# Performance work log

Hardware: AMD Instinct MI355X
Metric: run time of the kernel (lower is better)

The kernel has to match this reference:

```python
import jax, jax.numpy as jnp
import numpy as np

H, DH, DIM = 6, 13, 78   # heads, dim_head, model dim
LA, LG = 1.0, 0.5        # La (softmax scale), Lg (adjacency weight)
B, N = 16, 512


def setup_inputs() -> dict:
    key = jax.random.key(0)
    ks = jax.random.split(key, 5)
    x = jax.random.normal(ks[0], (B, N, DIM), jnp.float32)
    mask = jax.random.randint(ks[1], (B, N), 0, 2).astype(bool)
    adjacency_mat = jax.random.uniform(ks[2], (B, N, N), jnp.float32)
    # to_qkv: Linear(dim, 3*h*d, bias=False); to_out: Linear(h*d, dim)
    W_qkv = jax.random.normal(ks[3], (DIM, H * 3 * DH), jnp.float32) * 0.05
    W_out = jax.random.normal(ks[4], (H * DH, DIM), jnp.float32) * 0.05
    b_out = jnp.zeros((DIM,), jnp.float32)
    return {"x": x, "mask": mask, "adjacency_mat": adjacency_mat,
            "W_qkv": W_qkv, "W_out": W_out, "b_out": b_out}


def reference(x, mask, adjacency_mat, W_qkv, W_out, b_out):
    b, n, _ = x.shape
    # rearrange 'b n (h qkv d) -> b h n qkv d': inner dim split as (h, 3, d)
    qkv = (x @ W_qkv).reshape(b, n, H, 3, DH)
    qkv = jnp.transpose(qkv, (0, 2, 1, 3, 4))            # b h n 3 d
    q, k, v = qkv[..., 0, :], qkv[..., 1, :], qkv[..., 2, :]
    scale = DH ** -0.5
    dots = jnp.einsum('bhid,bhjd->bhij', q, k) * scale   # b h n n
    m = mask[:, None, :, None] & mask[:, None, None, :]  # b 1 n n
    big = jnp.finfo(dots.dtype).max
    dots = jnp.where(m, dots, -big)                      # masked_fill_(~mask, -max)
    adj = jnp.where(m, adjacency_mat[:, None, :, :], 0.0)
    attn = jax.nn.softmax(dots, axis=-1) * LA + LG * adj
    out = jnp.einsum('bhij,bhjd->bhid', attn, v)         # b h n d
    out = jnp.transpose(out, (0, 2, 1, 3)).reshape(b, n, H * DH)
    return out @ W_out + b_out
```

## Files before the change

kernel.cpp:

```cpp
#include <hip/hip_runtime.h>
#include <hip/hip_bf16.h>
#include <cfloat>

#define BB 16
#define NN 512
#define DIMX 78
#define NH 6
#define DHH 13
#define QS 16
#define KS 16
#define NC (NH*3*DHH)
#define SCALE 0.27735009811261457f
#define LAM_A 1.0f
#define LAM_G 0.5f
#define NU 32

typedef unsigned short ushortx;
typedef ushortx ushort8 __attribute__((ext_vector_type(8)));
typedef _Float16 halfx;
typedef halfx half2v __attribute__((ext_vector_type(2)));

__device__ __forceinline__ ushortx f2h(float f) {
  halfx h = (halfx)f;
  return __builtin_bit_cast(unsigned short, h);
}
__device__ __forceinline__ float h2lo(unsigned d) {
  return (float)__builtin_bit_cast(half2v, d).x;
}
__device__ __forceinline__ float h2hi(unsigned d) {
  return (float)__builtin_bit_cast(half2v, d).y;
}

__device__ __forceinline__ float dot2acc(unsigned qd, unsigned kd, float c) {
#if __has_builtin(__builtin_amdgcn_fdot2)
  return __builtin_amdgcn_fdot2(__builtin_bit_cast(half2v, qd),
                                __builtin_bit_cast(half2v, kd), c, false);
#else
  half2v qa = __builtin_bit_cast(half2v, qd);
  half2v ka = __builtin_bit_cast(half2v, kd);
  c = fmaf((float)qa.x, (float)ka.x, c);
  return fmaf((float)qa.y, (float)ka.y, c);
#endif
}

__global__ __launch_bounds__(256) void qkv_kernel(
    const float* __restrict__ x, const float* __restrict__ Wqkv,
    ushortx* __restrict__ qh, ushortx* __restrict__ kh, ushortx* __restrict__ vh) {
  int idx = blockIdx.x * 256 + threadIdx.x;
  const int NQ = 59;
  int rq = idx / NQ, cq = idx % NQ;
  if (rq >= (BB * NN) / 4) return;
  int c0 = cq * 4; if (c0 > NC - 4) c0 = NC - 4;
  int r0 = rq * 4;
  const float* x0 = x + (size_t)r0 * DIMX;
  const float* wb = Wqkv + c0;

  float acc[4][4];
#pragma unroll
  for (int r = 0; r < 4; ++r)
#pragma unroll
    for (int c = 0; c < 4; ++c) acc[r][c] = 0.f;

#pragma unroll 2
  for (int d0 = 0; d0 < 76; d0 += 4) {
    float2 wA[4], wB[4];
#pragma unroll
    for (int dd = 0; dd < 4; ++dd) {
      wA[dd] = *(const float2*)(wb + (d0 + dd) * NC);
      wB[dd] = *(const float2*)(wb + (d0 + dd) * NC + 2);
    }
    float2 xv[4][2];
#pragma unroll
    for (int r = 0; r < 4; ++r) {
      xv[r][0] = *(const float2*)(x0 + r * DIMX + d0);
      xv[r][1] = *(const float2*)(x0 + r * DIMX + d0 + 2);
    }
#pragma unroll
    for (int dd = 0; dd < 4; ++dd) {
#pragma unroll
      for (int r = 0; r < 4; ++r) {
        float xvv = (dd < 2) ? ((dd & 1) ? xv[r][0].y : xv[r][0].x)
                             : ((dd & 1) ? xv[r][1].y : xv[r][1].x);
        acc[r][0] = fmaf(xvv, wA[dd].x, acc[r][0]);
        acc[r][1] = fmaf(xvv, wA[dd].y, acc[r][1]);
        acc[r][2] = fmaf(xvv, wB[dd].x, acc[r][2]);
        acc[r][3] = fmaf(xvv, wB[dd].y, acc[r][3]);
      }
    }
  }
#pragma unroll
  for (int dd = 0; dd < 2; ++dd) {
    int d = 76 + dd;
    float2 wA = *(const float2*)(wb + d * NC);
    float2 wB = *(const float2*)(wb + d * NC + 2);
#pragma unroll
    for (int r = 0; r < 4; ++r) {
      float xvv = x0[r * DIMX + d];
      acc[r][0] = fmaf(xvv, wA.x, acc[r][0]);
      acc[r][1] = fmaf(xvv, wA.y, acc[r][1]);
      acc[r][2] = fmaf(xvv, wB.x, acc[r][2]);
      acc[r][3] = fmaf(xvv, wB.y, acc[r][3]);
    }
  }

#pragma unroll
  for (int r = 0; r < 4; ++r) {
    int bn = r0 + r;
    int b = bn / NN, n = bn % NN;
#pragma unroll
    for (int c = 0; c < 4; ++c) {
      int col = c0 + c;
      int h  = col / (3 * DHH);
      int rm = col % (3 * DHH);
      int t  = rm / DHH;
      int dd = rm % DHH;
      size_t rowb = ((size_t)b * NH + h) * NN + n;
      if (t == 0)      qh[rowb * QS + dd] = f2h(acc[r][c] * SCALE);
      else if (t == 1) kh[rowb * KS + dd] = f2h(acc[r][c]);
      else             vh[rowb * KS + dd] = f2h(acc[r][c]);
    }
  }
}

__global__ __launch_bounds__(256, 4) void attn_kernel(
    const ushortx* __restrict__ qh, const ushortx* __restrict__ kh,
    const ushortx* __restrict__ vh, const int* __restrict__ mask,
    const float* __restrict__ adj, float* __restrict__ att) {
  __shared__ uint4 k0s[NN], k1s[NN];
  __shared__ uint4 v0s[NN], v1s[NN];
  __shared__ __align__(16) unsigned qs[64][8];
  __shared__ short jact[NN];
  __shared__ unsigned char ract[64];
  __shared__ float vsum[DHH];
  __shared__ float vpart_s[2][DHH];
  __shared__ int nact_s, nract_s;

  int d0    = blockIdx.x;
  int orig  = (d0 & 7) * 96 + (d0 >> 3);
  int itile = orig & 7;
  int bh    = orig >> 3;
  int b     = bh / NH;
  int h     = bh % NH;
  int i0    = itile * 64;

  const ushortx* qb  = qh + (size_t)bh * NN * QS;
  const ushortx* kbb = kh + (size_t)bh * NN * KS;
  const ushortx* vbb = vh + (size_t)bh * NN * KS;
  const int* mrow = mask + b * NN;

  int tid  = threadIdx.x;
  int wave = tid >> 6, lane = tid & 63;

  if (wave == 0) {
    unsigned m8 = 0;
#pragma unroll
    for (int t = 0; t < 8; ++t) {
      int j = lane * 8 + t;
      if (mrow[j] != 0) m8 |= (1u << t);
    }
    int cnt = __popc(m8);
    int pre = cnt;
#pragma unroll
    for (int off = 1; off < 64; off <<= 1) {
      int o = __shfl_up(pre, off);
      if (lane >= off) pre += o;
    }
    pre -= cnt;
    int w = pre;
#pragma unroll
    for (int t = 0; t < 8; ++t)
      if ((m8 >> t) & 1) jact[w++] = (short)(lane * 8 + t);
    if (lane == 63) nact_s = pre + cnt;
  } else if (wave == 1) {
    int a = (mrow[i0 + lane] != 0) ? 1 : 0;
    int pre = a;
#pragma unroll
    for (int off = 1; off < 64; off <<= 1) {
      int o = __shfl_up(pre, off);
      if (lane >= off) pre += o;
    }
    pre -= a;
    if (a) ract[pre] = (unsigned char)lane;
    if (lane == 63) nract_s = pre + a;
  } else {
    int idx2 = (wave - 2) * 64 + lane;
    float vp[DHH];
#pragma unroll
    for (int d = 0; d < DHH; ++d) vp[d] = 0.f;
#pragma unroll
    for (int rep = 0; rep < 4; ++rep) {
      const ushortx* vr = vbb + (size_t)(idx2 + rep * 128) * KS;
      uint4 f0 = *(const uint4*)(vr);
      uint4 f1 = *(const uint4*)(vr + 8);
      vp[0] += h2lo(f0.x); vp[1] += h2hi(f0.x);
      vp[2] += h2lo(f0.y); vp[3] += h2hi(f0.y);
      vp[4] += h2lo(f0.z); vp[5] += h2hi(f0.z);
      vp[6] += h2lo(f0.w); vp[7] += h2hi(f0.w);
      vp[8] += h2lo(f1.x); vp[9] += h2hi(f1.x);
      vp[10] += h2lo(f1.y); vp[11] += h2hi(f1.y);
      vp[12] += h2lo(f1.z);
    }
#pragma unroll
    for (int off = 1; off < 64; off <<= 1)
#pragma unroll
      for (int d = 0; d < DHH; ++d) vp[d] += __shfl_xor(vp[d], off);
    if (lane < DHH) vpart_s[wave - 2][lane] = vp[lane];
  }
  __syncthreads();

  int na = nact_s;
  int nr = nract_s;

  {
    int r = tid >> 2, c2 = (tid & 3) * 2;
    *(uint2*)&qs[r][c2] = *(const uint2*)(qb + (size_t)(i0 + r) * QS + c2 * 2);
  }
  for (int t = tid; t < NN; t += 256) {
    if (t < na) {
      int j = jact[t];
      const ushortx* kr = kbb + (size_t)j * KS;
      const ushortx* vr = vbb + (size_t)j * KS;
      uint4 ka = *(const uint4*)(kr);
      uint4 kc = *(const uint4*)(kr + 8);
      kc.z &= 0xFFFFu;
      kc.w = 0;
      k0s[t] = ka;
      k1s[t] = kc;
      v0s[t] = *(const uint4*)(vr);
      v1s[t] = *(const uint4*)(vr + 8);
    } else {
      uint4 z = make_uint4(0, 0, 0, 0);
      k0s[t] = z; k1s[t] = z; v0s[t] = z; v1s[t] = z;
      jact[t] = 0;
    }
  }
  if (tid < DHH) vsum[tid] = vpart_s[0][tid] + vpart_s[1][tid];
  __syncthreads();

  for (int e = tid; e < 64 * DHH; e += 256) {
    int r = e / DHH, d = e % DHH;
    int i = i0 + r;
    if (mrow[i] == 0)
      att[((size_t)b * NN + i) * DIMX + h * DHH + d] = (LAM_A / 512.f) * vsum[d];
  }

  int grp = lane >> 4;
  int li  = lane & 15;

  for (int base = wave * 4; base < nr; base += 16) {
    int ridx = base + grp;
    bool rok = ridx < nr;
    int rl = ract[rok ? ridx : 0];
    int i  = i0 + rl;
    unsigned qd[7];
#pragma unroll
    for (int p = 0; p < 7; ++p) qd[p] = qs[rl][p];
    const float* adjr = adj + ((size_t)b * NN + i) * NN;

    float s[NU], aj[NU];
    float sum = 0.f;
#pragma unroll
    for (int u = 0; u < NU; ++u) {
      if (u * 16 < na) {
        int t = u * 16 + li;
        uint4 ka = k0s[t];
        uint4 kc = k1s[t];
        aj[u] = adjr[jact[t]];
        float dot = dot2acc(qd[0], ka.x, 0.f);
        dot = dot2acc(qd[1], ka.y, dot);
        dot = dot2acc(qd[2], ka.z, dot);
        dot = dot2acc(qd[3], ka.w, dot);
        dot = dot2acc(qd[4], kc.x, dot);
        dot = dot2acc(qd[5], kc.y, dot);
        dot = dot2acc(qd[6], kc.z, dot);
        float p = __expf((t < na) ? dot : -FLT_MAX);
        s[u] = p;
        sum += p;
      }
    }
#pragma unroll
    for (int off = 1; off < 16; off <<= 1) sum += __shfl_xor(sum, off);
    float inv = LAM_A / sum;

    float acc[DHH];
#pragma unroll
    for (int d = 0; d < DHH; ++d) acc[d] = 0.f;
#pragma unroll
    for (int u = 0; u < NU; ++u) {
      if (u * 16 < na) {
        int t = u * 16 + li;
        uint4 va = v0s[t];
        uint4 vc = v1s[t];
        float wu = fmaf(LAM_G, aj[u], s[u] * inv);
        acc[0]  = fmaf(h2lo(va.x), wu, acc[0]);
        acc[1]  = fmaf(h2hi(va.x), wu, acc[1]);
        acc[2]  = fmaf(h2lo(va.y), wu, acc[2]);
        acc[3]  = fmaf(h2hi(va.y), wu, acc[3]);
        acc[4]  = fmaf(h2lo(va.z), wu, acc[4]);
        acc[5]  = fmaf(h2hi(va.z), wu, acc[5]);
        acc[6]  = fmaf(h2lo(va.w), wu, acc[6]);
        acc[7]  = fmaf(h2hi(va.w), wu, acc[7]);
        acc[8]  = fmaf(h2lo(vc.x), wu, acc[8]);
        acc[9]  = fmaf(h2hi(vc.x), wu, acc[9]);
        acc[10] = fmaf(h2lo(vc.y), wu, acc[10]);
        acc[11] = fmaf(h2hi(vc.y), wu, acc[11]);
        acc[12] = fmaf(h2lo(vc.z), wu, acc[12]);
      }
    }
#pragma unroll
    for (int off = 1; off < 16; off <<= 1) {
#pragma unroll
      for (int d = 0; d < DHH; ++d) acc[d] += __shfl_xor(acc[d], off);
    }

    if (rok && li == 0) {
#pragma unroll
      for (int d = 0; d < DHH; ++d)
        att[((size_t)b * NN + i) * DIMX + h * DHH + d] = acc[d];
    }
  }
}

__global__ __launch_bounds__(320) void proj_kernel(
    const float* __restrict__ att, const float* __restrict__ Wout,
    const float* __restrict__ bout, float* __restrict__ out) {
  __shared__ float Ws[DIMX][80];
  __shared__ float as[32][82];
  __shared__ float bs[80];
  int tid = threadIdx.x;
  for (int e = tid; e < DIMX * 80; e += 320) {
    int r = e / 80, c = e % 80;
    Ws[r][c] = (c < DIMX) ? Wout[r * DIMX + c] : 0.f;
  }
  if (tid < 80) bs[tid] = (tid < DIMX) ? bout[tid] : 0.f;
  size_t row0 = (size_t)blockIdx.x * 32;
  for (int e = tid; e < 32 * DIMX; e += 320)
    as[e / DIMX][e % DIMX] = att[row0 * DIMX + e];
  __syncthreads();

  int r2 = tid / 20;
  int cq = tid % 20;
  int c0 = cq * 4;
  float acc0[4], acc1[4];
#pragma unroll
  for (int kk = 0; kk < 4; ++kk) { acc0[kk] = bs[c0 + kk]; acc1[kk] = bs[c0 + kk]; }

#pragma unroll 6
  for (int d = 0; d < DIMX; ++d) {
    float4 w = *(const float4*)&Ws[d][c0];
    float a0 = as[r2 * 2 + 0][d];
    float a1 = as[r2 * 2 + 1][d];
    acc0[0] = fmaf(a0, w.x, acc0[0]); acc0[1] = fmaf(a0, w.y, acc0[1]);
    acc0[2] = fmaf(a0, w.z, acc0[2]); acc0[3] = fmaf(a0, w.w, acc0[3]);
    acc1[0] = fmaf(a1, w.x, acc1[0]); acc1[1] = fmaf(a1, w.y, acc1[1]);
    acc1[2] = fmaf(a1, w.z, acc1[2]); acc1[3] = fmaf(a1, w.w, acc1[3]);
  }

  size_t r0o = (row0 + r2 * 2) * (size_t)DIMX;
  *(float2*)&out[r0o + c0]        = make_float2(acc0[0], acc0[1]);
  *(float2*)&out[r0o + DIMX + c0] = make_float2(acc1[0], acc1[1]);
  if (cq < 19) {
    *(float2*)&out[r0o + c0 + 2]        = make_float2(acc0[2], acc0[3]);
    *(float2*)&out[r0o + DIMX + c0 + 2] = make_float2(acc1[2], acc1[3]);
  }
}

extern "C" void kernel_launch(void* const* d_in, const int* in_sizes, int n_in,
                              void* d_out, int out_size, void* d_ws, size_t ws_size,
                              hipStream_t stream) {
  const float* x    = (const float*)d_in[0];
  const int*   mask = (const int*)d_in[1];
  const float* adj  = (const float*)d_in[2];
  const float* Wqkv = (const float*)d_in[3];
  const float* Wout = (const float*)d_in[4];
  const float* bout = (const float*)d_in[5];
  float* out = (float*)d_out;

  const size_t heads_rows = (size_t)BB * NH * NN;
  float*   att = (float*)d_ws;
  ushortx* qhp = (ushortx*)(att + (size_t)BB * NN * DIMX);
  ushortx* khp = qhp + heads_rows * QS;
  ushortx* vhp = khp + heads_rows * KS;

  const int NQ = 59;
  int qkv_threads = (BB * NN / 4) * NQ;
  qkv_kernel<<<(qkv_threads + 255) / 256, 256, 0, stream>>>(x, Wqkv, qhp, khp, vhp);
  attn_kernel<<<BB * NH * (NN / 64), 256, 0, stream>>>(qhp, khp, vhp, mask, adj, att);
  proj_kernel<<<BB * NN / 32, 320, 0, stream>>>(att, Wout, bout, out);
}
```

Before: 52.97 us.

## Fuse output projection into attention kernel via per-head atomic accumulation

Removes the separate projection kernel. The qkv kernel now also initializes the output with the bias, and each attention block multiplies its per-head 64x13 result by that head's slice of W_out and atomically adds it into the output. Fully masked rows use a precomputed projected mean-V vector. This drops the att intermediate round trip through global memory and one launch. In exchange it adds float atomics from 6 heads per output element, makes summation order nondeterministic, and lowers the occupancy hint to 3.

```diff
diff --git a/kernel.cpp b/kernel.cpp
--- a/kernel.cpp
+++ b/kernel.cpp
@@ -45,8 +45,13 @@
 
 __global__ __launch_bounds__(256) void qkv_kernel(
     const float* __restrict__ x, const float* __restrict__ Wqkv,
-    ushortx* __restrict__ qh, ushortx* __restrict__ kh, ushortx* __restrict__ vh) {
+    const float* __restrict__ bout,
+    ushortx* __restrict__ qh, ushortx* __restrict__ kh, ushortx* __restrict__ vh,
+    float* __restrict__ out) {
   int idx = blockIdx.x * 256 + threadIdx.x;
+  for (int e = idx; e < BB * NN * DIMX; e += gridDim.x * 256)
+    out[e] = bout[e % DIMX];
+
   const int NQ = 59;
   int rq = idx / NQ, cq = idx % NQ;
   if (rq >= (BB * NN) / 4) return;
@@ -122,13 +127,17 @@
   }
 }
 
-__global__ __launch_bounds__(256, 4) void attn_kernel(
+__global__ __launch_bounds__(256, 3) void attn_kernel(
     const ushortx* __restrict__ qh, const ushortx* __restrict__ kh,
     const ushortx* __restrict__ vh, const int* __restrict__ mask,
-    const float* __restrict__ adj, float* __restrict__ att) {
+    const float* __restrict__ adj, const float* __restrict__ Wout,
+    float* __restrict__ out) {
   __shared__ uint4 k0s[NN], k1s[NN];
   __shared__ uint4 v0s[NN], v1s[NN];
   __shared__ __align__(16) unsigned qs[64][8];
+  __shared__ float att_s[64][14];
+  __shared__ float Ws2[DHH][80];
+  __shared__ float uv[80];
   __shared__ short jact[NN];
   __shared__ unsigned char ract[64];
   __shared__ float vsum[DHH];
@@ -214,6 +223,10 @@
   {
     int r = tid >> 2, c2 = (tid & 3) * 2;
     *(uint2*)&qs[r][c2] = *(const uint2*)(qb + (size_t)(i0 + r) * QS + c2 * 2);
+  }
+  for (int e = tid; e < DHH * 80; e += 256) {
+    int r = e / 80, c = e % 80;
+    Ws2[r][c] = (c < DIMX) ? Wout[(h * DHH + r) * DIMX + c] : 0.f;
   }
   for (int t = tid; t < NN; t += 256) {
     if (t < na) {
@@ -237,11 +250,11 @@
   if (tid < DHH) vsum[tid] = vpart_s[0][tid] + vpart_s[1][tid];
   __syncthreads();
 
-  for (int e = tid; e < 64 * DHH; e += 256) {
-    int r = e / DHH, d = e % DHH;
-    int i = i0 + r;
-    if (mrow[i] == 0)
-      att[((size_t)b * NN + i) * DIMX + h * DHH + d] = (LAM_A / 512.f) * vsum[d];
+  if (tid < DIMX) {
+    float a = 0.f;
+#pragma unroll
+    for (int d = 0; d < DHH; ++d) a = fmaf(vsum[d], Ws2[d][tid], a);
+    uv[tid] = (LAM_A / 512.f) * a;
   }
 
   int grp = lane >> 4;
@@ -315,53 +328,24 @@
 
     if (rok && li == 0) {
 #pragma unroll
-      for (int d = 0; d < DHH; ++d)
-        att[((size_t)b * NN + i) * DIMX + h * DHH + d] = acc[d];
-    }
-  }
-}
-
-__global__ __launch_bounds__(320) void proj_kernel(
-    const float* __restrict__ att, const float* __restrict__ Wout,
-    const float* __restrict__ bout, float* __restrict__ out) {
-  __shared__ float Ws[DIMX][80];
-  __shared__ float as[32][82];
-  __shared__ float bs[80];
-  int tid = threadIdx.x;
-  for (int e = tid; e < DIMX * 80; e += 320) {
-    int r = e / 80, c = e % 80;
-    Ws[r][c] = (c < DIMX) ? Wout[r * DIMX + c] : 0.f;
-  }
-  if (tid < 80) bs[tid] = (tid < DIMX) ? bout[tid] : 0.f;
-  size_t row0 = (size_t)blockIdx.x * 32;
-  for (int e = tid; e < 32 * DIMX; e += 320)
-    as[e / DIMX][e % DIMX] = att[row0 * DIMX + e];
+      for (int d = 0; d < DHH; ++d) att_s[rl][d] = acc[d];
+    }
+  }
+
   __syncthreads();
-
-  int r2 = tid / 20;
-  int cq = tid % 20;
-  int c0 = cq * 4;
-  float acc0[4], acc1[4];
-#pragma unroll
-  for (int kk = 0; kk < 4; ++kk) { acc0[kk] = bs[c0 + kk]; acc1[kk] = bs[c0 + kk]; }
-
-#pragma unroll 6
-  for (int d = 0; d < DIMX; ++d) {
-    float4 w = *(const float4*)&Ws[d][c0];
-    float a0 = as[r2 * 2 + 0][d];
-    float a1 = as[r2 * 2 + 1][d];
-    acc0[0] = fmaf(a0, w.x, acc0[0]); acc0[1] = fmaf(a0, w.y, acc0[1]);
-    acc0[2] = fmaf(a0, w.z, acc0[2]); acc0[3] = fmaf(a0, w.w, acc0[3]);
-    acc1[0] = fmaf(a1, w.x, acc1[0]); acc1[1] = fmaf(a1, w.y, acc1[1]);
-    acc1[2] = fmaf(a1, w.z, acc1[2]); acc1[3] = fmaf(a1, w.w, acc1[3]);
-  }
-
-  size_t r0o = (row0 + r2 * 2) * (size_t)DIMX;
-  *(float2*)&out[r0o + c0]        = make_float2(acc0[0], acc0[1]);
-  *(float2*)&out[r0o + DIMX + c0] = make_float2(acc1[0], acc1[1]);
-  if (cq < 19) {
-    *(float2*)&out[r0o + c0 + 2]        = make_float2(acc0[2], acc0[3]);
-    *(float2*)&out[r0o + DIMX + c0 + 2] = make_float2(acc1[2], acc1[3]);
+  for (int e = tid; e < 64 * DIMX; e += 256) {
+    int r = e / DIMX, c = e % DIMX;
+    int i = i0 + r;
+    float val;
+    if (mrow[i] == 0) {
+      val = uv[c];
+    } else {
+      float a = 0.f;
+#pragma unroll
+      for (int d = 0; d < DHH; ++d) a = fmaf(att_s[r][d], Ws2[d][c], a);
+      val = a;
+    }
+    atomicAdd(&out[((size_t)b * NN + i) * DIMX + c], val);
   }
 }
 
@@ -377,14 +361,14 @@
   float* out = (float*)d_out;
 
   const size_t heads_rows = (size_t)BB * NH * NN;
-  float*   att = (float*)d_ws;
-  ushortx* qhp = (ushortx*)(att + (size_t)BB * NN * DIMX);
+  ushortx* qhp = (ushortx*)d_ws;
   ushortx* khp = qhp + heads_rows * QS;
   ushortx* vhp = khp + heads_rows * KS;
 
   const int NQ = 59;
   int qkv_threads = (BB * NN / 4) * NQ;
-  qkv_kernel<<<(qkv_threads + 255) / 256, 256, 0, stream>>>(x, Wqkv, qhp, khp, vhp);
-  attn_kernel<<<BB * NH * (NN / 64), 256, 0, stream>>>(qhp, khp, vhp, mask, adj, att);
-  proj_kernel<<<BB * NN / 32, 320, 0, stream>>>(att, Wout, bout, out);
-}
+  qkv_kernel<<<(qkv_threads + 255) / 256, 256, 0, stream>>>(x, Wqkv, bout,
+                                                            qhp, khp, vhp, out);
+  attn_kernel<<<BB * NH * (NN / 64), 256, 0, stream>>>(qhp, khp, vhp, mask,
+                                                       adj, Wout, out);
+}
```

After: 57.60 us. 8.7% more time.

## Precompact adjacency columns by mask in a separate kernel before attention

Applied to the files above, without the earlier changes.

Adds a kernel that, for each batch, compacts every adjacency row so that only the columns with an active mask are stored contiguously in a workspace buffer. The attention kernel then reads this compacted row with contiguous per-lane loads instead of gathering through the active-index list. This is meant to replace scattered gather loads of the adjacency matrix, which is read once per head, with coalesced loads. In exchange it adds one extra kernel that reads the full adjacency tensor and writes a compacted copy of similar size, plus a larger workspace. Padded slots past the active count are never written, so reads there pick up stale values, although they only reach lanes that should already be masked.

```diff
diff --git a/kernel.cpp b/kernel.cpp
--- a/kernel.cpp
+++ b/kernel.cpp
@@ -43,6 +43,50 @@
 #endif
 }
 
+__global__ __launch_bounds__(256) void adjc_kernel(
+    const int* __restrict__ mask, const float* __restrict__ adj,
+    float* __restrict__ adjc) {
+  __shared__ short jpos[NN];
+  int blk = blockIdx.x;
+  int b   = blk >> 5;
+  int i0  = (blk & 31) * 16;
+  const int* mrow = mask + b * NN;
+  int tid = threadIdx.x, wave = tid >> 6, lane = tid & 63;
+
+  if (wave == 0) {
+    unsigned m8 = 0;
+#pragma unroll
+    for (int t = 0; t < 8; ++t) {
+      int j = lane * 8 + t;
+      if (mrow[j] != 0) m8 |= (1u << t);
+    }
+    int cnt = __popc(m8);
+    int pre = cnt;
+#pragma unroll
+    for (int off = 1; off < 64; off <<= 1) {
+      int o = __shfl_up(pre, off);
+      if (lane >= off) pre += o;
+    }
+    pre -= cnt;
+    int w = pre;
+#pragma unroll
+    for (int t = 0; t < 8; ++t) {
+      int j = lane * 8 + t;
+      jpos[j] = ((m8 >> t) & 1) ? (short)(w++) : (short)-1;
+    }
+  }
+  __syncthreads();
+
+  const float* arow = adj + ((size_t)b * NN + i0) * NN;
+  float* crow = adjc + ((size_t)b * NN + i0) * NN;
+  for (int e = tid; e < 16 * NN; e += 256) {
+    int r = e >> 9, j = e & (NN - 1);
+    float v = arow[(size_t)r * NN + j];
+    short p = jpos[j];
+    if (p >= 0) crow[(size_t)r * NN + p] = v;
+  }
+}
+
 __global__ __launch_bounds__(256) void qkv_kernel(
     const float* __restrict__ x, const float* __restrict__ Wqkv,
     ushortx* __restrict__ qh, ushortx* __restrict__ kh, ushortx* __restrict__ vh) {
@@ -125,7 +169,7 @@
 __global__ __launch_bounds__(256, 4) void attn_kernel(
     const ushortx* __restrict__ qh, const ushortx* __restrict__ kh,
     const ushortx* __restrict__ vh, const int* __restrict__ mask,
-    const float* __restrict__ adj, float* __restrict__ att) {
+    const float* __restrict__ adjc, float* __restrict__ att) {
   __shared__ uint4 k0s[NN], k1s[NN];
   __shared__ uint4 v0s[NN], v1s[NN];
   __shared__ __align__(16) unsigned qs[64][8];
@@ -231,7 +275,6 @@
     } else {
       uint4 z = make_uint4(0, 0, 0, 0);
       k0s[t] = z; k1s[t] = z; v0s[t] = z; v1s[t] = z;
-      jact[t] = 0;
     }
   }
   if (tid < DHH) vsum[tid] = vpart_s[0][tid] + vpart_s[1][tid];
@@ -255,7 +298,7 @@
     unsigned qd[7];
 #pragma unroll
     for (int p = 0; p < 7; ++p) qd[p] = qs[rl][p];
-    const float* adjr = adj + ((size_t)b * NN + i) * NN;
+    const float* adjcr = adjc + ((size_t)b * NN + i) * NN;
 
     float s[NU], aj[NU];
     float sum = 0.f;
@@ -265,7 +308,7 @@
         int t = u * 16 + li;
         uint4 ka = k0s[t];
         uint4 kc = k1s[t];
-        aj[u] = adjr[jact[t]];
+        aj[u] = adjcr[t];
         float dot = dot2acc(qd[0], ka.x, 0.f);
         dot = dot2acc(qd[1], ka.y, dot);
         dot = dot2acc(qd[2], ka.z, dot);
@@ -377,14 +420,17 @@
   float* out = (float*)d_out;
 
   const size_t heads_rows = (size_t)BB * NH * NN;
-  float*   att = (float*)d_ws;
-  ushortx* qhp = (ushortx*)(att + (size_t)BB * NN * DIMX);
-  ushortx* khp = qhp + heads_rows * QS;
-  ushortx* vhp = khp + heads_rows * KS;
+  float*   att  = (float*)d_ws;
+  float*   adjc = att + (size_t)BB * NN * DIMX;
+  ushortx* qhp  = (ushortx*)(adjc + (size_t)BB * NN * NN);
+  ushortx* khp  = qhp + heads_rows * QS;
+  ushortx* vhp  = khp + heads_rows * KS;
 
   const int NQ = 59;
   int qkv_threads = (BB * NN / 4) * NQ;
+  adjc_kernel<<<BB * 32, 256, 0, stream>>>(mask, adj, adjc);
   qkv_kernel<<<(qkv_threads + 255) / 256, 256, 0, stream>>>(x, Wqkv, qhp, khp, vhp);
-  attn_kernel<<<BB * NH * (NN / 64), 256, 0, stream>>>(qhp, khp, vhp, mask, adj, att);
+  attn_kernel<<<BB * NH * (NN / 64), 256, 0, stream>>>(qhp, khp, vhp, mask,
+                                                       adjc, att);
   proj_kernel<<<BB * NN / 32, 320, 0, stream>>>(att, Wout, bout, out);
 }
```

After: 67.47 us. 1.27x slower.
